# Optimization experiments

Measured on AMD Instinct MI355X. Metric: run time of the kernel, lower is better.

Reference implementation:

```python
import jax, jax.numpy as jnp
import numpy as np

GX, GY, NH = 480, 360, 32
EPS = 1e-5


def _bn(x, g, b):
    # torch BatchNorm1d training-mode stats over the point dimension
    m = jnp.mean(x, axis=0)
    v = jnp.mean((x - m) ** 2, axis=0)
    return g * (x - m) / jnp.sqrt(v + EPS) + b


def setup_inputs():
    key = jax.random.key(0)
    ks = jax.random.split(key, 24)
    B, N, F = 2, 120000, 7
    s = 0.02
    inp = {
        "pt_fea": jax.random.normal(ks[0], (B, N, F), jnp.float32),
        "xy_ind": jax.random.randint(ks[1], (B, N, 2), 0, 360, dtype=jnp.int32),
        "bn0_g": jnp.ones((7,), jnp.float32), "bn0_b": jnp.zeros((7,), jnp.float32),
        "W1": jax.random.normal(ks[2], (7, 64), jnp.float32) * s,  "b1": jnp.zeros((64,), jnp.float32),
        "bn1_g": jnp.ones((64,), jnp.float32), "bn1_b": jnp.zeros((64,), jnp.float32),
        "W2": jax.random.normal(ks[3], (64, 128), jnp.float32) * s, "b2": jnp.zeros((128,), jnp.float32),
        "bn2_g": jnp.ones((128,), jnp.float32), "bn2_b": jnp.zeros((128,), jnp.float32),
        "W3": jax.random.normal(ks[4], (128, 256), jnp.float32) * s, "b3": jnp.zeros((256,), jnp.float32),
        "bn3_g": jnp.ones((256,), jnp.float32), "bn3_b": jnp.zeros((256,), jnp.float32),
        "W4": jax.random.normal(ks[5], (256, 512), jnp.float32) * s, "b4": jnp.zeros((512,), jnp.float32),
        "W5": jax.random.normal(ks[6], (512, NH), jnp.float32) * s, "b5": jnp.zeros((NH,), jnp.float32),
    }
    return inp


def _forward_sample(fea, xy, bn0_g, bn0_b, W1, b1, bn1_g, bn1_b, W2, b2,
                    bn2_g, bn2_b, W3, b3, bn3_g, bn3_b, W4, b4, W5, b5):
    # Simplified PointNet: BN -> (Linear, BN, ReLU) x3 -> Linear
    x = _bn(fea, bn0_g, bn0_b)
    x = jax.nn.relu(_bn(x @ W1 + b1, bn1_g, bn1_b))
    x = jax.nn.relu(_bn(x @ W2 + b2, bn2_g, bn2_b))
    x = jax.nn.relu(_bn(x @ W3 + b3, bn3_g, bn3_b))
    x = x @ W4 + b4                              # [N, 512]
    # per-voxel segment max over flattened BEV cell id
    ids = xy[:, 0] * GY + xy[:, 1]               # [N]
    nseg = GX * GY
    seg = jax.ops.segment_max(x, ids, num_segments=nseg)   # [nseg, 512]
    cnt = jax.ops.segment_sum(jnp.ones(ids.shape[0], x.dtype), ids, num_segments=nseg)
    occ = (cnt > 0)[:, None]
    seg = jnp.where(occ, seg, 0.0)               # empty voxels -> 0 (scatter semantics)
    nh = jax.nn.relu(seg @ W5 + b5)              # fea_compression
    nh = jnp.where(occ, nh, 0.0)
    return nh.reshape(GX, GY, NH).transpose(2, 0, 1)  # [NH, GX, GY]


def reference(pt_fea, xy_ind, bn0_g, bn0_b, W1, b1, bn1_g, bn1_b, W2, b2,
              bn2_g, bn2_b, W3, b3, bn3_g, bn3_b, W4, b4, W5, b5):
    f = lambda fea, xy: _forward_sample(fea, xy, bn0_g, bn0_b, W1, b1, bn1_g, bn1_b,
                                        W2, b2, bn2_g, bn2_b, W3, b3, bn3_g, bn3_b,
                                        W4, b4, W5, b5)
    return jax.vmap(f)(pt_fea, xy_ind)           # [B, NH, GX, GY]
```

## Files before the change

kernel.cpp:

```cpp
#include <hip/hip_runtime.h>
#include <cstdint>

#define GXD 480
#define GYD 360
#define NHD 32
#define NPTS 120000
#define MPAD 120064
#define MB128 (MPAD/128)
#define SEGR 129600
#define NSEG (GXD*GYD)
#define EPSB 1e-5f

using short8 = __attribute__((ext_vector_type(8))) short;
using f32x4  = __attribute__((ext_vector_type(4))) float;

__device__ __forceinline__ float bf2f(unsigned short u) {
    return __uint_as_float(((unsigned int)u) << 16);
}
__device__ __forceinline__ unsigned short f2bf(float f) {
    unsigned int u = __float_as_uint(f);
    u += 0x7fffu + ((u >> 16) & 1u);
    return (unsigned short)(u >> 16);
}
__device__ __forceinline__ unsigned int bnrelu_pack(unsigned int wv, float sc0, float sh0,
                                                    float sc1, float sh1)
{
    float lo = __uint_as_float(wv << 16);
    float hi = __uint_as_float(wv & 0xffff0000u);
    lo = fmaxf(fmaf(lo, sc0, sh0), 0.f);
    hi = fmaxf(fmaf(hi, sc1, sh1), 0.f);
    unsigned int r;
    asm("v_cvt_pk_bf16_f32 %0, %1, %2" : "=v"(r) : "v"(lo), "v"(hi));
    return r;
}
__device__ __forceinline__ unsigned int pk_bf16(float lo, float hi)
{
    unsigned int r;
    asm("v_cvt_pk_bf16_f32 %0, %1, %2" : "=v"(r) : "v"(lo), "v"(hi));
    return r;
}
__device__ __forceinline__ short8 bn_frag(short8 a, float4 s0, float4 s1,
                                          float4 h0, float4 h1)
{
    union { short8 v; uint4 u; } in, out;
    in.v = a;
    out.u.x = bnrelu_pack(in.u.x, s0.x, h0.x, s0.y, h0.y);
    out.u.y = bnrelu_pack(in.u.y, s0.z, h0.z, s0.w, h0.w);
    out.u.z = bnrelu_pack(in.u.z, s1.x, h1.x, s1.y, h1.y);
    out.u.w = bnrelu_pack(in.u.w, s1.z, h1.z, s1.w, h1.w);
    return out.v;
}

__device__ __forceinline__ void async16(const unsigned short* g, unsigned short* l)
{
    __builtin_amdgcn_global_load_lds(
        (const __attribute__((address_space(1))) unsigned int*)g,
        (__attribute__((address_space(3))) unsigned int*)l, 16, 0, 0);
}

__global__ __launch_bounds__(256) void bn0_stats_kernel(
    const float* __restrict__ fea, float* __restrict__ s0, float* __restrict__ q0)
{
    float s[7] = {0,0,0,0,0,0,0}, q[7] = {0,0,0,0,0,0,0};
    for (int p = blockIdx.x * 256 + threadIdx.x; p < NPTS; p += gridDim.x * 256) {
        const float* r = fea + (size_t)p * 7;
#pragma unroll
        for (int f = 0; f < 7; ++f) { float v = r[f]; s[f] += v; q[f] += v * v; }
    }
    __shared__ float red[256];
    int t = threadIdx.x;
#pragma unroll
    for (int f = 0; f < 7; ++f) {
        red[t] = s[f]; __syncthreads();
        for (int o = 128; o > 0; o >>= 1) {
            if (t < o) red[t] += red[t + o];
            __syncthreads();
        }
        if (t == 0) atomicAdd(&s0[f], red[0]);
        __syncthreads();
        red[t] = q[f]; __syncthreads();
        for (int o = 128; o > 0; o >>= 1) {
            if (t < o) red[t] += red[t + o];
            __syncthreads();
        }
        if (t == 0) atomicAdd(&q0[f], red[0]);
        __syncthreads();
    }
}

__global__ void prep0_kernel(const float* __restrict__ s0, const float* __restrict__ q0,
                             const float* __restrict__ g0, const float* __restrict__ b0,
                             const float* __restrict__ W1, const float* __restrict__ b1,
                             float* __restrict__ W1p, float* __restrict__ b1p)
{
    __shared__ float sc[7], sh[7];
    int t = threadIdx.x;
    if (t < 7) {
        float m = s0[t] / (float)NPTS;
        float v = q0[t] / (float)NPTS - m * m;
        float inv = 1.0f / sqrtf(fmaxf(v, 0.f) + EPSB);
        sc[t] = g0[t] * inv;
        sh[t] = b0[t] - m * g0[t] * inv;
    }
    __syncthreads();
    if (t < 64) {
        float acc = b1[t];
#pragma unroll
        for (int f = 0; f < 7; ++f) {
            W1p[f * 64 + t] = W1[f * 64 + t] * sc[f];
            acc += sh[f] * W1[f * 64 + t];
        }
        b1p[t] = acc;
    }
}

__global__ __launch_bounds__(256) void wtrans_kernel(const float* __restrict__ W,
                                                     unsigned short* __restrict__ Wt,
                                                     int K, int N)
{
    int i = blockIdx.x * 256 + threadIdx.x;
    if (i < K * N) {
        int k = i / N, n = i % N;
        Wt[(size_t)n * K + k] = f2bf(W[i]);
    }
}

__global__ __launch_bounds__(256) void layer1_kernel(
    const float* __restrict__ fea, const float* __restrict__ W1p, const float* __restrict__ b1p,
    unsigned short* __restrict__ y1, float* __restrict__ sum1, float* __restrict__ sq1)
{
    __shared__ float Wl[448], bl[64];
    __shared__ float feaL[256 * 7];
    __shared__ float colsum[64], colsq[64];
    int t = threadIdx.x;
    int p0 = blockIdx.x * 256;
    for (int i = t; i < 448; i += 256) Wl[i] = W1p[i];
    if (t < 64) { bl[t] = b1p[t]; colsum[t] = 0.f; colsq[t] = 0.f; }
    int nval7 = (NPTS - p0) * 7;
    for (int i = t; i < 256 * 7; i += 256)
        feaL[i] = (i < nval7) ? fea[(size_t)p0 * 7 + i] : 0.f;
    __syncthreads();
    int cg = t & 7, pt = t >> 3;
    float s[8] = {}, q[8] = {};
#pragma unroll
    for (int it = 0; it < 8; ++it) {
        int row = it * 32 + pt;
        bool valid = (p0 + row) < NPTS;
        float f[7];
#pragma unroll
        for (int ff = 0; ff < 7; ++ff) f[ff] = feaL[row * 7 + ff];
        float vj[8];
#pragma unroll
        for (int j = 0; j < 8; ++j) {
            int c = cg * 8 + j;
            float v = bl[c];
#pragma unroll
            for (int ff = 0; ff < 7; ++ff) v = fmaf(f[ff], Wl[ff * 64 + c], v);
            vj[j] = v;
            if (valid) { s[j] += v; q[j] += v * v; }
        }
        uint4 ow;
        ow.x = (unsigned int)f2bf(vj[0]) | ((unsigned int)f2bf(vj[1]) << 16);
        ow.y = (unsigned int)f2bf(vj[2]) | ((unsigned int)f2bf(vj[3]) << 16);
        ow.z = (unsigned int)f2bf(vj[4]) | ((unsigned int)f2bf(vj[5]) << 16);
        ow.w = (unsigned int)f2bf(vj[6]) | ((unsigned int)f2bf(vj[7]) << 16);
        *(uint4*)(y1 + (size_t)(p0 + row) * 64 + cg * 8) = ow;
    }
#pragma unroll
    for (int off = 8; off < 64; off <<= 1) {
#pragma unroll
        for (int j = 0; j < 8; ++j) {
            s[j] += __shfl_xor(s[j], off);
            q[j] += __shfl_xor(q[j], off);
        }
    }
    if ((t & 63) < 8) {
#pragma unroll
        for (int j = 0; j < 8; ++j) {
            atomicAdd(&colsum[cg * 8 + j], s[j]);
            atomicAdd(&colsq[cg * 8 + j], q[j]);
        }
    }
    __syncthreads();
    if (t < 64) {
        atomicAdd(&sum1[t], colsum[t]);
        atomicAdd(&sq1[t], colsq[t]);
    }
}

template<int K, int NC, bool STATS>
__global__ __launch_bounds__(256) void gemm_quad(
    const unsigned short* __restrict__ A, const unsigned short* __restrict__ Wt,
    const float* __restrict__ bsum, const float* __restrict__ bsq,
    const float* __restrict__ bg, const float* __restrict__ bb,
    const float* __restrict__ bias, unsigned short* __restrict__ Y,
    float* __restrict__ osum, float* __restrict__ osq)
{
    __shared__ __align__(16) unsigned short lds[16384];
    __shared__ __align__(16) float scs[K], shs[K];
    __shared__ float colsum[128], colsq[128];
    int t = threadIdx.x;
    int w = t >> 6, ln = t & 63, quad = ln >> 4, lr = ln & 15;
    int wr = w >> 1, wc = w & 1;
    const int mbase = blockIdx.y * 128;
    const int cbase = blockIdx.x * 128;
    unsigned short* Asl = lds;
    unsigned short* Bsl = lds + 8192;

    for (int i = t; i < K; i += 256) {
        float m = bsum[i] / (float)NPTS;
        float v = bsq[i] / (float)NPTS - m * m;
        float inv = 1.0f / sqrtf(fmaxf(v, 0.f) + EPSB);
        scs[i] = bg[i] * inv;
        shs[i] = bb[i] - m * bg[i] * inv;
    }
    if (STATS && t < 128) { colsum[t] = 0.f; colsq[t] = 0.f; }
    __syncthreads();

    const int srow = w * 16 + (ln >> 2);
    const int koff = (ln & 3) * 8;

    auto stage = [&](int buf, int kt) {
#pragma unroll
        for (int half = 0; half < 2; ++half) {
            int row = half * 64 + srow;
            async16(A  + (size_t)(mbase + row) * K + kt + koff,
                    Asl + buf * 4096 + half * 2048 + w * 512 + ln * 8);
            async16(Wt + (size_t)(cbase + row) * K + kt + koff,
                    Bsl + buf * 4096 + half * 2048 + w * 512 + ln * 8);
        }
    };

    f32x4 acc[4][4];
#pragma unroll
    for (int i = 0; i < 4; ++i)
#pragma unroll
        for (int j = 0; j < 4; ++j) acc[i][j] = (f32x4){0.f, 0.f, 0.f, 0.f};

    stage(0, 0);
    stage(1, 32);

    constexpr int NR = K / 32;
#pragma unroll
    for (int r = 0; r < NR; ++r) {
        const int buf = r & 1;
        if (r + 1 < NR)
            asm volatile("s_waitcnt vmcnt(4)" ::: "memory");
        else
            asm volatile("s_waitcnt vmcnt(0)" ::: "memory");
        asm volatile("s_barrier" ::: "memory");
        short8 af[4], bfr[4];
#pragma unroll
        for (int mi = 0; mi < 4; ++mi)
            af[mi] = *(const short8*)&Asl[buf * 4096 + (wr * 64 + mi * 16 + lr) * 32 + quad * 8];
#pragma unroll
        for (int ni = 0; ni < 4; ++ni)
            bfr[ni] = *(const short8*)&Bsl[buf * 4096 + (wc * 64 + ni * 16 + lr) * 32 + quad * 8];
        const int k0 = r * 32 + quad * 8;
        float4 s0 = *(const float4*)&scs[k0];
        float4 s1 = *(const float4*)&scs[k0 + 4];
        float4 h0 = *(const float4*)&shs[k0];
        float4 h1 = *(const float4*)&shs[k0 + 4];
        asm volatile("s_waitcnt lgkmcnt(0)" ::: "memory");
        asm volatile("s_barrier" ::: "memory");
        if (r + 2 < NR)
            stage(buf, (r + 2) * 32);
#pragma unroll
        for (int mi = 0; mi < 4; ++mi)
            af[mi] = bn_frag(af[mi], s0, s1, h0, h1);
#pragma unroll
        for (int mi = 0; mi < 4; ++mi)
#pragma unroll
            for (int ni = 0; ni < 4; ++ni)
                acc[mi][ni] = __builtin_amdgcn_mfma_f32_16x16x32_bf16(
                    af[mi], bfr[ni], acc[mi][ni], 0, 0, 0);
    }
    __syncthreads();

    unsigned short* Cw = lds + w * 4096;
#pragma unroll
    for (int ni = 0; ni < 4; ++ni) {
        int col = ni * 16 + lr;
        float bv = bias[cbase + wc * 64 + col];
        float s = 0.f, q = 0.f;
#pragma unroll
        for (int mi = 0; mi < 4; ++mi) {
            int rb = mi * 16 + quad * 4;
#pragma unroll
            for (int r = 0; r < 4; ++r) {
                float v = acc[mi][ni][r] + bv;
                Cw[(rb + r) * 64 + col] = f2bf(v);
                if (STATS && (mbase + wr * 64 + rb + r) < NPTS) { s += v; q += v * v; }
            }
        }
        if (STATS) {
            atomicAdd(&colsum[wc * 64 + col], s);
            atomicAdd(&colsq[wc * 64 + col], q);
        }
    }
#pragma unroll
    for (int i = 0; i < 8; ++i) {
        int idx = i * 64 + ln;
        int row = idx >> 3, colq = (idx & 7) * 8;
        *(uint4*)(Y + (size_t)(mbase + wr * 64 + row) * NC + cbase + wc * 64 + colq) =
            *(const uint4*)&Cw[row * 64 + colq];
    }
    if (STATS) {
        __syncthreads();
        if (t < 128) {
            atomicAdd(&osum[blockIdx.x * 128 + t], colsum[t]);
            atomicAdd(&osq[blockIdx.x * 128 + t], colsq[t]);
        }
    }
}

__global__ __launch_bounds__(256) void hist_kernel(const int* __restrict__ xy,
                                                   int* __restrict__ cnt)
{
    int p = blockIdx.x * 256 + threadIdx.x;
    if (p < NPTS) {
        int id = xy[(size_t)p * 2] * GYD + xy[(size_t)p * 2 + 1];
        atomicAdd(&cnt[id], 1);
    }
}

__global__ __launch_bounds__(256) void scanA_kernel(const int* __restrict__ cnt,
                                                    int* __restrict__ csum)
{
    __shared__ int red[256];
    int t = threadIdx.x, base = blockIdx.x * 2048;
    int s = 0;
    for (int i = t; i < 2048; i += 256) {
        int idx = base + i;
        if (idx < SEGR) s += cnt[idx];
    }
    red[t] = s; __syncthreads();
    for (int o = 128; o > 0; o >>= 1) { if (t < o) red[t] += red[t + o]; __syncthreads(); }
    if (t == 0) csum[blockIdx.x] = red[0];
}

__global__ void scanB_kernel(int* __restrict__ csum, int* __restrict__ offs)
{
    if (threadIdx.x == 0) {
        int run = 0;
        for (int i = 0; i < 64; ++i) { int v = csum[i]; csum[i] = run; run += v; }
        offs[SEGR] = run;
    }
}

__global__ __launch_bounds__(256) void scanC_kernel(const int* __restrict__ cnt,
                                                    const int* __restrict__ csum,
                                                    int* __restrict__ offs,
                                                    int* __restrict__ cursor)
{
    __shared__ int red[256];
    int t = threadIdx.x, base = blockIdx.x * 2048;
    int v[8]; int s = 0;
#pragma unroll
    for (int i = 0; i < 8; ++i) {
        int idx = base + t * 8 + i;
        v[i] = (idx < SEGR) ? cnt[idx] : 0;
        s += v[i];
    }
    red[t] = s; __syncthreads();
    for (int o = 1; o < 256; o <<= 1) {
        int x = (t >= o) ? red[t - o] : 0;
        __syncthreads();
        red[t] += x;
        __syncthreads();
    }
    int run = red[t] - s + csum[blockIdx.x];
#pragma unroll
    for (int i = 0; i < 8; ++i) {
        int idx = base + t * 8 + i;
        if (idx < SEGR) { offs[idx] = run; cursor[idx] = run; }
        run += v[i];
    }
}

__global__ __launch_bounds__(256) void scatter_idx_kernel(const int* __restrict__ xy,
                                                          int* __restrict__ cursor,
                                                          int* __restrict__ order)
{
    int p = blockIdx.x * 256 + threadIdx.x;
    if (p < NPTS) {
        int id = xy[(size_t)p * 2] * GYD + xy[(size_t)p * 2 + 1];
        int pos = atomicAdd(&cursor[id], 1);
        order[pos] = p;
    }
}

__global__ __launch_bounds__(256) void l4seg_kernel(
    const unsigned short* __restrict__ y3, const unsigned short* __restrict__ Wt4,
    const float* __restrict__ b4, const unsigned short* __restrict__ Wt5,
    const float* __restrict__ b5, const int* __restrict__ offs,
    const int* __restrict__ ord,
    const float* __restrict__ bsum, const float* __restrict__ bsq,
    const float* __restrict__ bg, const float* __restrict__ bb,
    float* __restrict__ out)
{
    __shared__ __align__(16) unsigned short Bsl[64 * 256];
    __shared__ __align__(16) unsigned short w5s[32 * 64];
    __shared__ __align__(16) unsigned short y4s[64 * 72];
    __shared__ float b4s[512];
    __shared__ float scs[256], shs[256];
    __shared__ int offs_s[65];
    __shared__ int osl[128];
    int t = threadIdx.x;
    int w = t >> 6, ln = t & 63, quad = ln >> 4, lr = ln & 15;
    int c0 = blockIdx.x * 64;
    if (t < 65) offs_s[t] = offs[c0 + t];
    for (int i = t; i < 512; i += 256) b4s[i] = b4[i];
    __syncthreads();
    const int jb = offs_s[0], je = offs_s[64];
    if (jb == je) {
#pragma unroll
        for (int j = 0; j < 8; ++j)
            out[(size_t)(w * 8 + j) * NSEG + c0 + ln] = 0.f;
        return;
    }
    {
        float m = bsum[t] / (float)NPTS;
        float v = bsq[t] / (float)NPTS - m * m;
        float inv = 1.0f / sqrtf(fmaxf(v, 0.f) + EPSB);
        scs[t] = bg[t] * inv;
        shs[t] = bb[t] - m * bg[t] * inv;
    }
    if (t < 128) { int aj = jb + t; osl[t] = (aj < je) ? ord[aj] : 0; }
    __syncthreads();

    const int cell = t >> 2, q = t & 3;
    const int cjb = offs_s[cell], cje = offs_s[cell + 1];
    const int nch = (je - jb + 63) >> 6;

    short8 af0[8], af1[8];
    {
        int j0 = w * 16 + lr; if (jb + j0 >= je) j0 = je - 1 - jb;
        const unsigned short* Ar0 = y3 + (size_t)osl[j0] * 256 + quad * 8;
#pragma unroll
        for (int r = 0; r < 8; ++r) af0[r] = *(const short8*)(Ar0 + r * 32);
        int j1 = 64 + w * 16 + lr; if (jb + j1 >= je) j1 = je - 1 - jb;
        const unsigned short* Ar1 = y3 + (size_t)osl[j1] * 256 + quad * 8;
#pragma unroll
        for (int r = 0; r < 8; ++r) af1[r] = *(const short8*)(Ar1 + r * 32);
#pragma unroll
        for (int r = 0; r < 8; ++r) {
            const int k0 = r * 32 + quad * 8;
            float4 s0 = *(const float4*)&scs[k0];
            float4 s1 = *(const float4*)&scs[k0 + 4];
            float4 h0 = *(const float4*)&shs[k0];
            float4 h1 = *(const float4*)&shs[k0 + 4];
            af0[r] = bn_frag(af0[r], s0, s1, h0, h1);
            af1[r] = bn_frag(af1[r], s0, s1, h0, h1);
        }
    }

    f32x4 eacc[2];
    eacc[0] = (f32x4){0.f, 0.f, 0.f, 0.f};
    eacc[1] = (f32x4){0.f, 0.f, 0.f, 0.f};

    auto stageB = [&](int p) {
#pragma unroll
        for (int i = 0; i < 8; ++i) {
            int rl = w * 16 + i * 2 + (ln >> 5);
            int cl = (ln & 31) ^ (rl & 7);
            async16(Wt4 + (size_t)(p * 64 + rl) * 256 + cl * 8,
                    Bsl + (w * 16 + i * 2) * 256 + ln * 8);
        }
    };
    auto stageW5 = [&](int p) {
        int rl = t >> 3, cl = (t & 7) ^ (rl & 7);
        async16(Wt5 + (size_t)rl * 512 + p * 64 + cl * 8, w5s + t * 8);
    };
    auto mfma_chunk = [&](const short8* af, f32x4* acc) {
#pragma unroll
        for (int r = 0; r < 8; ++r) {
            const int cp = (r * 4 + quad) ^ (lr & 7);
#pragma unroll
            for (int ni = 0; ni < 4; ++ni) {
                short8 bfr = *(const short8*)&Bsl[(ni * 16 + lr) * 256 + cp * 8];
                acc[ni] = __builtin_amdgcn_mfma_f32_16x16x32_bf16(af[r], bfr, acc[ni], 0, 0, 0);
            }
        }
    };

    stageB(0); stageW5(0);

    for (int p = 0; p < 8; ++p) {
        asm volatile("s_waitcnt vmcnt(0)" ::: "memory");
        asm volatile("s_barrier" ::: "memory");
        float mxv[16];
#pragma unroll
        for (int i = 0; i < 16; ++i) mxv[i] = -3.0e38f;

        for (int c = 0; c < nch; ++c) {
            const int cs = jb + c * 64;
            f32x4 acc[4];
#pragma unroll
            for (int i = 0; i < 4; ++i) acc[i] = (f32x4){0.f, 0.f, 0.f, 0.f};
            if (c == 0) {
                mfma_chunk(af0, acc);
            } else if (c == 1) {
                mfma_chunk(af1, acc);
            } else {
                int j = cs + w * 16 + lr; if (j >= je) j = je - 1;
                const unsigned short* Ar = y3 + (size_t)ord[j] * 256 + quad * 8;
#pragma unroll
                for (int r = 0; r < 8; ++r) {
                    short8 a = *(const short8*)(Ar + r * 32);
                    const int k0 = r * 32 + quad * 8;
                    float4 s0 = *(const float4*)&scs[k0];
                    float4 s1 = *(const float4*)&scs[k0 + 4];
                    float4 h0 = *(const float4*)&shs[k0];
                    float4 h1 = *(const float4*)&shs[k0 + 4];
                    a = bn_frag(a, s0, s1, h0, h1);
                    const int cp = (r * 4 + quad) ^ (lr & 7);
#pragma unroll
                    for (int ni = 0; ni < 4; ++ni) {
                        short8 bfr = *(const short8*)&Bsl[(ni * 16 + lr) * 256 + cp * 8];
                        acc[ni] = __builtin_amdgcn_mfma_f32_16x16x32_bf16(a, bfr, acc[ni], 0, 0, 0);
                    }
                }
            }
#pragma unroll
            for (int ni = 0; ni < 4; ++ni) {
                float bv = b4s[p * 64 + ni * 16 + lr];
#pragma unroll
                for (int rr = 0; rr < 4; ++rr)
                    y4s[(w * 16 + quad * 4 + rr) * 72 + ni * 16 + lr] = f2bf(acc[ni][rr] + bv);
            }
            asm volatile("s_waitcnt lgkmcnt(0)" ::: "memory");
            asm volatile("s_barrier" ::: "memory");
            if (c == nch - 1 && p < 7)
                stageB(p + 1);
            int lo = cjb > cs ? cjb : cs;
            int hi = cje < cs + 64 ? cje : cs + 64;
            for (int jj = lo; jj < hi; ++jj) {
                const uint4* rp = (const uint4*)&y4s[(jj - cs) * 72 + q * 16];
                uint4 v0 = rp[0], v1 = rp[1];
                unsigned int wv[8] = {v0.x, v0.y, v0.z, v0.w, v1.x, v1.y, v1.z, v1.w};
#pragma unroll
                for (int k2 = 0; k2 < 8; ++k2) {
                    mxv[2 * k2]     = fmaxf(mxv[2 * k2],     bf2f((unsigned short)(wv[k2] & 0xffffu)));
                    mxv[2 * k2 + 1] = fmaxf(mxv[2 * k2 + 1], bf2f((unsigned short)(wv[k2] >> 16)));
                }
            }
            asm volatile("s_barrier" ::: "memory");
        }
        {
            bool empty = (cjb == cje);
#pragma unroll
            for (int i = 0; i < 8; ++i) {
                float lo2 = empty ? 0.f : mxv[2 * i], hi2 = empty ? 0.f : mxv[2 * i + 1];
                *(unsigned int*)&y4s[cell * 72 + q * 16 + 2 * i] = pk_bf16(lo2, hi2);
            }
        }
        asm volatile("s_waitcnt lgkmcnt(0)" ::: "memory");
        asm volatile("s_barrier" ::: "memory");
#pragma unroll
        for (int kt = 0; kt < 2; ++kt) {
            short8 af2 = *(const short8*)&y4s[(w * 16 + lr) * 72 + kt * 32 + quad * 8];
            const int cp = (kt * 4 + quad) ^ (lr & 7);
#pragma unroll
            for (int ni = 0; ni < 2; ++ni) {
                short8 bfr = *(const short8*)&w5s[(ni * 16 + lr) * 64 + cp * 8];
                eacc[ni] = __builtin_amdgcn_mfma_f32_16x16x32_bf16(af2, bfr, eacc[ni], 0, 0, 0);
            }
        }
        asm volatile("s_waitcnt lgkmcnt(0)" ::: "memory");
        asm volatile("s_barrier" ::: "memory");
        if (p < 7) stageW5(p + 1);
    }
    float* outs = (float*)&Bsl[0];
#pragma unroll
    for (int ni = 0; ni < 2; ++ni) {
        int h = ni * 16 + lr;
        float bv = b5[h];
#pragma unroll
        for (int rr = 0; rr < 4; ++rr) {
            int cr = w * 16 + quad * 4 + rr;
            bool oc = offs_s[cr + 1] > offs_s[cr];
            outs[cr * 33 + h] = oc ? fmaxf(eacc[ni][rr] + bv, 0.f) : 0.f;
        }
    }
    __syncthreads();
#pragma unroll
    for (int j = 0; j < 8; ++j)
        out[(size_t)(w * 8 + j) * NSEG + c0 + ln] = outs[ln * 33 + w * 8 + j];
}

__global__ __launch_bounds__(256) void ztail_kernel(float* __restrict__ out)
{
    int i = blockIdx.x * 256 + threadIdx.x;
    const int per = (NSEG - SEGR) / 4;
    int h = i / per, c = i % per;
    *(float4*)(out + (size_t)h * NSEG + SEGR + (size_t)c * 4) = make_float4(0.f, 0.f, 0.f, 0.f);
}

extern "C" void kernel_launch(void* const* d_in, const int* in_sizes, int n_in,
                              void* d_out, int out_size, void* d_ws, size_t ws_size,
                              hipStream_t stream)
{
    const float* pt_fea = (const float*)d_in[0];
    const int*   xy_ind = (const int*)d_in[1];
    const float* bn0_g  = (const float*)d_in[2];
    const float* bn0_b  = (const float*)d_in[3];
    const float* W1     = (const float*)d_in[4];
    const float* b1     = (const float*)d_in[5];
    const float* bn1_g  = (const float*)d_in[6];
    const float* bn1_b  = (const float*)d_in[7];
    const float* W2     = (const float*)d_in[8];
    const float* b2     = (const float*)d_in[9];
    const float* bn2_g  = (const float*)d_in[10];
    const float* bn2_b  = (const float*)d_in[11];
    const float* W3     = (const float*)d_in[12];
    const float* b3     = (const float*)d_in[13];
    const float* bn3_g  = (const float*)d_in[14];
    const float* bn3_b  = (const float*)d_in[15];
    const float* W4     = (const float*)d_in[16];
    const float* b4     = (const float*)d_in[17];
    const float* W5     = (const float*)d_in[18];
    const float* b5     = (const float*)d_in[19];
    float* out = (float*)d_out;

    const size_t oY2   = 61472768;
    const size_t oE    = oY2 + (size_t)MPAD * 128 * 2;
    const size_t oCnt  = oE + (size_t)SEGR * 32 * 4;
    const size_t oOffs = oCnt + 518400;
    const size_t oCur  = oOffs + 518528;
    const size_t oOrd  = oCur + 518400;
    const size_t oCsum = oOrd + 480000;
    const size_t oSt   = oCsum + 512;
    const size_t oWt2  = oSt + 16384;
    const size_t oWt3  = oWt2 + 16384;
    const size_t oWt4  = oWt3 + 65536;
    const size_t oWt5  = oWt4 + 262144;

    unsigned short* y1   = (unsigned short*)d_ws;
    unsigned short* y3   = (unsigned short*)d_ws;
    unsigned short* y2   = (unsigned short*)((char*)d_ws + oY2);
    int*            cnt  = (int*)((char*)d_ws + oCnt);
    int*            offs = (int*)((char*)d_ws + oOffs);
    int*            cur  = (int*)((char*)d_ws + oCur);
    int*            ord  = (int*)((char*)d_ws + oOrd);
    int*            csum = (int*)((char*)d_ws + oCsum);
    float*          st   = (float*)((char*)d_ws + oSt);
    unsigned short* Wt2  = (unsigned short*)((char*)d_ws + oWt2);
    unsigned short* Wt3  = (unsigned short*)((char*)d_ws + oWt3);
    unsigned short* Wt4  = (unsigned short*)((char*)d_ws + oWt4);
    unsigned short* Wt5  = (unsigned short*)((char*)d_ws + oWt5);

    float* s0 = st + 0;     float* q0 = st + 8;
    float* W1p = st + 16;   float* b1p = st + 464;
    float* sum1 = st + 528; float* sq1 = st + 592;
    float* sum2 = st + 784; float* sq2 = st + 912;
    float* sum3 = st + 1296; float* sq3 = st + 1552;

    wtrans_kernel<<<(64 * 128 + 255) / 256, 256, 0, stream>>>(W2, Wt2, 64, 128);
    wtrans_kernel<<<(128 * 256 + 255) / 256, 256, 0, stream>>>(W3, Wt3, 128, 256);
    wtrans_kernel<<<(256 * 512 + 255) / 256, 256, 0, stream>>>(W4, Wt4, 256, 512);
    wtrans_kernel<<<(512 * 32 + 255) / 256, 256, 0, stream>>>(W5, Wt5, 512, 32);

    for (int b = 0; b < 2; ++b) {
        const float* fea_b = pt_fea + (size_t)b * NPTS * 7;
        const int*   xy_b  = xy_ind + (size_t)b * NPTS * 2;
        float*       out_b = out + (size_t)b * NHD * NSEG;

        (void)hipMemsetAsync(st, 0, 2320 * sizeof(float), stream);
        (void)hipMemsetAsync(cnt, 0, (size_t)SEGR * 4, stream);

        bn0_stats_kernel<<<128, 256, 0, stream>>>(fea_b, s0, q0);
        prep0_kernel<<<1, 64, 0, stream>>>(s0, q0, bn0_g, bn0_b, W1, b1, W1p, b1p);
        layer1_kernel<<<MPAD / 256, 256, 0, stream>>>(fea_b, W1p, b1p, y1, sum1, sq1);
        gemm_quad<64, 128, true><<<dim3(1, MB128), 256, 0, stream>>>(
            y1, Wt2, sum1, sq1, bn1_g, bn1_b, b2, y2, sum2, sq2);
        gemm_quad<128, 256, true><<<dim3(2, MB128), 256, 0, stream>>>(
            y2, Wt3, sum2, sq2, bn2_g, bn2_b, b3, y3, sum3, sq3);

        hist_kernel<<<(NPTS + 255) / 256, 256, 0, stream>>>(xy_b, cnt);
        scanA_kernel<<<64, 256, 0, stream>>>(cnt, csum);
        scanB_kernel<<<1, 64, 0, stream>>>(csum, offs);
        scanC_kernel<<<64, 256, 0, stream>>>(cnt, csum, offs, cur);
        scatter_idx_kernel<<<(NPTS + 255) / 256, 256, 0, stream>>>(xy_b, cur, ord);

        l4seg_kernel<<<SEGR / 64, 256, 0, stream>>>(
            y3, Wt4, b4, Wt5, b5, offs, ord, sum3, sq3, bn3_g, bn3_b, out_b);
        ztail_kernel<<<1350, 256, 0, stream>>>(out_b);
    }
}
```

Before: 738.5 us.

## Process 128 cells per block and feed segment-max results directly into W5 MFMA

Each l4seg block now covers 128 BEV cells instead of 64, halving the block count and the number of times the Wt4 and Wt5 weight tiles are streamed per point chunk. Each lane now keeps running maxima for two cells laid out in MFMA A-fragment order. The maxima are packed straight into registers for the W5 MFMA, which removes the round trip through shared memory and two barriers. Per-lane register pressure roughly doubles and grid parallelism halves, which may lower occupancy or leave the tail of the grid underfilled.

```diff
diff --git a/kernel.cpp b/kernel.cpp
--- a/kernel.cpp
+++ b/kernel.cpp
@@ -404,19 +404,24 @@
     __shared__ __align__(16) unsigned short y4s[64 * 72];
     __shared__ float b4s[512];
     __shared__ float scs[256], shs[256];
-    __shared__ int offs_s[65];
+    __shared__ int offs_s[129];
     __shared__ int osl[128];
     int t = threadIdx.x;
     int w = t >> 6, ln = t & 63, quad = ln >> 4, lr = ln & 15;
-    int c0 = blockIdx.x * 64;
-    if (t < 65) offs_s[t] = offs[c0 + t];
+    const int c0 = blockIdx.x * 128;
+    if (t < 129) { int ci = c0 + t; offs_s[t] = offs[ci < SEGR ? ci : SEGR]; }
     for (int i = t; i < 512; i += 256) b4s[i] = b4[i];
     __syncthreads();
-    const int jb = offs_s[0], je = offs_s[64];
+    const int jb = offs_s[0], je = offs_s[128];
     if (jb == je) {
 #pragma unroll
-        for (int j = 0; j < 8; ++j)
-            out[(size_t)(w * 8 + j) * NSEG + c0 + ln] = 0.f;
+        for (int m = 0; m < 2; ++m) {
+            int cell = m * 64 + ln;
+            if (c0 + cell < SEGR)
+#pragma unroll
+                for (int j = 0; j < 8; ++j)
+                    out[(size_t)(w * 8 + j) * NSEG + c0 + cell] = 0.f;
+        }
         return;
     }
     {
@@ -426,21 +431,20 @@
         scs[t] = bg[t] * inv;
         shs[t] = bb[t] - m * bg[t] * inv;
     }
-    if (t < 128) { int aj = jb + t; osl[t] = (aj < je) ? ord[aj] : 0; }
+    if (t < 128) { int aj = jb + t; osl[t] = ord[aj < je ? aj : je - 1]; }
     __syncthreads();
 
-    const int cell = t >> 2, q = t & 3;
-    const int cjb = offs_s[cell], cje = offs_s[cell + 1];
+    const int cellA = w * 16 + lr, cellB = 64 + w * 16 + lr;
+    const int cjbA = offs_s[cellA], cjeA = offs_s[cellA + 1];
+    const int cjbB = offs_s[cellB], cjeB = offs_s[cellB + 1];
     const int nch = (je - jb + 63) >> 6;
 
     short8 af0[8], af1[8];
     {
-        int j0 = w * 16 + lr; if (jb + j0 >= je) j0 = je - 1 - jb;
-        const unsigned short* Ar0 = y3 + (size_t)osl[j0] * 256 + quad * 8;
+        const unsigned short* Ar0 = y3 + (size_t)osl[w * 16 + lr] * 256 + quad * 8;
 #pragma unroll
         for (int r = 0; r < 8; ++r) af0[r] = *(const short8*)(Ar0 + r * 32);
-        int j1 = 64 + w * 16 + lr; if (jb + j1 >= je) j1 = je - 1 - jb;
-        const unsigned short* Ar1 = y3 + (size_t)osl[j1] * 256 + quad * 8;
+        const unsigned short* Ar1 = y3 + (size_t)osl[64 + w * 16 + lr] * 256 + quad * 8;
 #pragma unroll
         for (int r = 0; r < 8; ++r) af1[r] = *(const short8*)(Ar1 + r * 32);
 #pragma unroll
@@ -455,9 +459,11 @@
         }
     }
 
-    f32x4 eacc[2];
-    eacc[0] = (f32x4){0.f, 0.f, 0.f, 0.f};
-    eacc[1] = (f32x4){0.f, 0.f, 0.f, 0.f};
+    f32x4 eacc[2][2];
+#pragma unroll
+    for (int m = 0; m < 2; ++m)
+#pragma unroll
+        for (int ni = 0; ni < 2; ++ni) eacc[m][ni] = (f32x4){0.f, 0.f, 0.f, 0.f};
 
     auto stageB = [&](int p) {
 #pragma unroll
@@ -489,9 +495,9 @@
     for (int p = 0; p < 8; ++p) {
         asm volatile("s_waitcnt vmcnt(0)" ::: "memory");
         asm volatile("s_barrier" ::: "memory");
-        float mxv[16];
-#pragma unroll
-        for (int i = 0; i < 16; ++i) mxv[i] = -3.0e38f;
+        float mxvA[16], mxvB[16];
+#pragma unroll
+        for (int i = 0; i < 16; ++i) { mxvA[i] = -3.0e38f; mxvB[i] = -3.0e38f; }
 
         for (int c = 0; c < nch; ++c) {
             const int cs = jb + c * 64;
@@ -533,38 +539,54 @@
             asm volatile("s_barrier" ::: "memory");
             if (c == nch - 1 && p < 7)
                 stageB(p + 1);
-            int lo = cjb > cs ? cjb : cs;
-            int hi = cje < cs + 64 ? cje : cs + 64;
-            for (int jj = lo; jj < hi; ++jj) {
-                const uint4* rp = (const uint4*)&y4s[(jj - cs) * 72 + q * 16];
-                uint4 v0 = rp[0], v1 = rp[1];
-                unsigned int wv[8] = {v0.x, v0.y, v0.z, v0.w, v1.x, v1.y, v1.z, v1.w};
-#pragma unroll
-                for (int k2 = 0; k2 < 8; ++k2) {
-                    mxv[2 * k2]     = fmaxf(mxv[2 * k2],     bf2f((unsigned short)(wv[k2] & 0xffffu)));
-                    mxv[2 * k2 + 1] = fmaxf(mxv[2 * k2 + 1], bf2f((unsigned short)(wv[k2] >> 16)));
+            {
+                int lo = cjbA > cs ? cjbA : cs;
+                int hi = cjeA < cs + 64 ? cjeA : cs + 64;
+                for (int jj = lo; jj < hi; ++jj) {
+#pragma unroll
+                    for (int kt = 0; kt < 2; ++kt) {
+                        const uint4 v = *(const uint4*)&y4s[(jj - cs) * 72 + kt * 32 + quad * 8];
+                        unsigned int wv[4] = {v.x, v.y, v.z, v.w};
+#pragma unroll
+                        for (int k2 = 0; k2 < 4; ++k2) {
+                            mxvA[kt * 8 + 2 * k2]     = fmaxf(mxvA[kt * 8 + 2 * k2],     bf2f((unsigned short)(wv[k2] & 0xffffu)));
+                            mxvA[kt * 8 + 2 * k2 + 1] = fmaxf(mxvA[kt * 8 + 2 * k2 + 1], bf2f((unsigned short)(wv[k2] >> 16)));
+                        }
+                    }
+                }
+                lo = cjbB > cs ? cjbB : cs;
+                hi = cjeB < cs + 64 ? cjeB : cs + 64;
+                for (int jj = lo; jj < hi; ++jj) {
+#pragma unroll
+                    for (int kt = 0; kt < 2; ++kt) {
+                        const uint4 v = *(const uint4*)&y4s[(jj - cs) * 72 + kt * 32 + quad * 8];
+                        unsigned int wv[4] = {v.x, v.y, v.z, v.w};
+#pragma unroll
+                        for (int k2 = 0; k2 < 4; ++k2) {
+                            mxvB[kt * 8 + 2 * k2]     = fmaxf(mxvB[kt * 8 + 2 * k2],     bf2f((unsigned short)(wv[k2] & 0xffffu)));
+                            mxvB[kt * 8 + 2 * k2 + 1] = fmaxf(mxvB[kt * 8 + 2 * k2 + 1], bf2f((unsigned short)(wv[k2] >> 16)));
+                        }
+                    }
                 }
             }
-            asm volatile("s_barrier" ::: "memory");
-        }
-        {
-            bool empty = (cjb == cje);
-#pragma unroll
-            for (int i = 0; i < 8; ++i) {
-                float lo2 = empty ? 0.f : mxv[2 * i], hi2 = empty ? 0.f : mxv[2 * i + 1];
-                *(unsigned int*)&y4s[cell * 72 + q * 16 + 2 * i] = pk_bf16(lo2, hi2);
+            if (c + 1 < nch)
+                asm volatile("s_barrier" ::: "memory");
+        }
+        const bool emptyA = (cjbA == cjeA), emptyB = (cjbB == cjeB);
+#pragma unroll
+        for (int kt = 0; kt < 2; ++kt) {
+            union { short8 v; unsigned int u[4]; } sa, sb;
+#pragma unroll
+            for (int j = 0; j < 4; ++j) {
+                sa.u[j] = emptyA ? 0u : pk_bf16(mxvA[kt * 8 + 2 * j], mxvA[kt * 8 + 2 * j + 1]);
+                sb.u[j] = emptyB ? 0u : pk_bf16(mxvB[kt * 8 + 2 * j], mxvB[kt * 8 + 2 * j + 1]);
             }
-        }
-        asm volatile("s_waitcnt lgkmcnt(0)" ::: "memory");
-        asm volatile("s_barrier" ::: "memory");
-#pragma unroll
-        for (int kt = 0; kt < 2; ++kt) {
-            short8 af2 = *(const short8*)&y4s[(w * 16 + lr) * 72 + kt * 32 + quad * 8];
             const int cp = (kt * 4 + quad) ^ (lr & 7);
 #pragma unroll
             for (int ni = 0; ni < 2; ++ni) {
                 short8 bfr = *(const short8*)&w5s[(ni * 16 + lr) * 64 + cp * 8];
-                eacc[ni] = __builtin_amdgcn_mfma_f32_16x16x32_bf16(af2, bfr, eacc[ni], 0, 0, 0);
+                eacc[0][ni] = __builtin_amdgcn_mfma_f32_16x16x32_bf16(sa.v, bfr, eacc[0][ni], 0, 0, 0);
+                eacc[1][ni] = __builtin_amdgcn_mfma_f32_16x16x32_bf16(sb.v, bfr, eacc[1][ni], 0, 0, 0);
             }
         }
         asm volatile("s_waitcnt lgkmcnt(0)" ::: "memory");
@@ -573,20 +595,27 @@
     }
     float* outs = (float*)&Bsl[0];
 #pragma unroll
-    for (int ni = 0; ni < 2; ++ni) {
-        int h = ni * 16 + lr;
-        float bv = b5[h];
-#pragma unroll
-        for (int rr = 0; rr < 4; ++rr) {
-            int cr = w * 16 + quad * 4 + rr;
-            bool oc = offs_s[cr + 1] > offs_s[cr];
-            outs[cr * 33 + h] = oc ? fmaxf(eacc[ni][rr] + bv, 0.f) : 0.f;
-        }
-    }
+    for (int m = 0; m < 2; ++m)
+#pragma unroll
+        for (int ni = 0; ni < 2; ++ni) {
+            int h = ni * 16 + lr;
+            float bv = b5[h];
+#pragma unroll
+            for (int rr = 0; rr < 4; ++rr) {
+                int cr = m * 64 + w * 16 + quad * 4 + rr;
+                bool oc = offs_s[cr + 1] > offs_s[cr];
+                outs[cr * 33 + h] = oc ? fmaxf(eacc[m][ni][rr] + bv, 0.f) : 0.f;
+            }
+        }
     __syncthreads();
 #pragma unroll
-    for (int j = 0; j < 8; ++j)
-        out[(size_t)(w * 8 + j) * NSEG + c0 + ln] = outs[ln * 33 + w * 8 + j];
+    for (int m = 0; m < 2; ++m) {
+        int cell = m * 64 + ln;
+        if (c0 + cell < SEGR)
+#pragma unroll
+            for (int j = 0; j < 8; ++j)
+                out[(size_t)(w * 8 + j) * NSEG + c0 + cell] = outs[cell * 33 + w * 8 + j];
+    }
 }
 
 __global__ __launch_bounds__(256) void ztail_kernel(float* __restrict__ out)
@@ -683,7 +712,7 @@
         scanC_kernel<<<64, 256, 0, stream>>>(cnt, csum, offs, cur);
         scatter_idx_kernel<<<(NPTS + 255) / 256, 256, 0, stream>>>(xy_b, cur, ord);
 
-        l4seg_kernel<<<SEGR / 64, 256, 0, stream>>>(
+        l4seg_kernel<<<(SEGR + 127) / 128, 256, 0, stream>>>(
             y3, Wt4, b4, Wt5, b5, offs, ord, sum3, sq3, bn3_g, bn3_b, out_b);
         ztail_kernel<<<1350, 256, 0, stream>>>(out_b);
     }
```

Result: no change. 742.2 us (+0.5%).
